# Kernel optimization log

Measured on AMD Instinct MI355X. Metric: run time of the kernel, lower is better.

The kernel has to match this reference:

```python
import jax, jax.numpy as jnp
import numpy as np

B, P, N, E, F = 1024, 64, 512, 256, 64

def setup_inputs() -> dict:
    key = jax.random.key(0)
    ks = jax.random.split(key, 10)
    return {
        'feasible_personal_info_nodes': jax.random.uniform(ks[0], (B, P), dtype=jnp.float32),
        'workers_decision': jax.random.uniform(ks[1], (B, P, 2), dtype=jnp.float32),
        'known_one_hot': jax.random.uniform(ks[2], (B, P, F), dtype=jnp.float32),
        'unknown_one_hot': jax.random.uniform(ks[3], (B, P, F), dtype=jnp.float32),
        'known_differ_one_hot': jax.random.uniform(ks[4], (B, P, F), dtype=jnp.float32),
        'total_qa_turn_one_hot': jax.random.uniform(ks[5], (B, F), dtype=jnp.float32),
        'personal_nodes': jax.random.randint(ks[6], (B, P), 0, N, dtype=jnp.int64) if jax.config.jax_enable_x64 else jax.random.randint(ks[6], (B, P), 0, N, dtype=jnp.int32),
        'final_node_embed': jax.random.normal(ks[7], (B, N, E), dtype=jnp.float32),
        'W': jax.random.normal(ks[8], (E, E), dtype=jnp.float32) * 0.02,
        'b': jax.random.normal(ks[9], (E,), dtype=jnp.float32) * 0.02,
    }

def reference(feasible_personal_info_nodes, workers_decision, known_one_hot,
              unknown_one_hot, known_differ_one_hot, total_qa_turn_one_hot,
              personal_nodes, final_node_embed, W, b):
    batch_size, personal_node_num = personal_nodes.shape
    # batch_embedding_lookup: gather node rows per batch -> (B, P, E)
    personal_node_embed = jnp.take_along_axis(
        final_node_embed, personal_nodes[:, :, None], axis=1)
    # Linear + Tanh
    transferred = jnp.tanh(jnp.einsum('bpe,ef->bpf', personal_node_embed, W) + b)
    # msg_agg == 'avg'
    agg_state = jnp.sum(transferred, axis=1) / personal_node_num
    manager_state = jnp.concatenate((
        feasible_personal_info_nodes,
        workers_decision.reshape(batch_size, -1),
        known_one_hot.reshape(batch_size, -1),
        unknown_one_hot.reshape(batch_size, -1),
        known_differ_one_hot.reshape(batch_size, -1),
        total_qa_turn_one_hot,
        agg_state), axis=1)
    return manager_state
```

## Files before the change

### kernel.cpp

```cpp
#include <hip/hip_runtime.h>
#include <hip/hip_bf16.h>
#include <math.h>

#define BB 1024
#define PP 64
#define NN 512
#define EE 256


#define LDA 264

typedef short bf16x8 __attribute__((ext_vector_type(8)));
typedef float f32x4  __attribute__((ext_vector_type(4)));

__device__ inline unsigned short f2bf(float x) {
    union { float f; unsigned int u; } v; v.f = x;
    unsigned int r = (v.u + 0x7FFFu + ((v.u >> 16) & 1u)) >> 16;
    return (unsigned short)r;
}

__global__ void wconv_kernel(const float* __restrict__ W,
                             unsigned short* __restrict__ Wt) {
    int i = blockIdx.x * blockDim.x + threadIdx.x;
    int k = i >> 8;
    int f = i & 255;
    int t = f >> 4;
    int c = k >> 5;
    int kk = k & 31;
    int lane = (kk >> 3) * 16 + (f & 15);
    int dst = (((t * 8 + c) * 64) + lane) * 8 + (kk & 7);
    Wt[dst] = f2bf(W[i]);
}

__global__ void fused_kernel(
    const float* __restrict__ feas, const float* __restrict__ workers,
    const float* __restrict__ known, const float* __restrict__ unknown,
    const float* __restrict__ differ, const float* __restrict__ qa,
    const int* __restrict__ pn, const float* __restrict__ embed,
    const float* __restrict__ bias, const unsigned short* __restrict__ Wt,
    float* __restrict__ out)
{
    if (blockIdx.x < BB) {
        __shared__ unsigned short sA[PP * LDA];
        const int b = blockIdx.x;
        const int tid = threadIdx.x;

        {
            const int p = tid >> 2, q = tid & 3;
            const int idx = pn[b * PP + p];
            const float4* src =
                (const float4*)(embed + ((size_t)b * NN + idx) * EE) + q * 16;
            unsigned short* dst = sA + p * LDA + q * 64;
            #pragma unroll
            for (int i = 0; i < 16; ++i) {
                float4 v = src[i];
                dst[i * 4 + 0] = f2bf(v.x);
                dst[i * 4 + 1] = f2bf(v.y);
                dst[i * 4 + 2] = f2bf(v.z);
                dst[i * 4 + 3] = f2bf(v.w);
            }
        }
        __syncthreads();

        const int wave = tid >> 6, lane = tid & 63;
        const int m = lane & 15, quad = lane >> 4;

        f32x4 acc[4][4];
        #pragma unroll
        for (int mt = 0; mt < 4; ++mt)
            #pragma unroll
            for (int ft = 0; ft < 4; ++ft)
                acc[mt][ft] = (f32x4){0.f, 0.f, 0.f, 0.f};

        #pragma unroll
        for (int c = 0; c < 8; ++c) {
            bf16x8 aF[4], bF[4];
            #pragma unroll
            for (int mt = 0; mt < 4; ++mt) {
                const unsigned short* ap =
                    sA + (mt * 16 + m) * LDA + c * 32 + quad * 8;
                aF[mt] = *(const bf16x8*)ap;
            }
            #pragma unroll
            for (int ft = 0; ft < 4; ++ft) {
                const int t = wave * 4 + ft;
                const unsigned short* bp = Wt + (((t * 8 + c) * 64) + lane) * 8;
                bF[ft] = *(const bf16x8*)bp;
            }
            #pragma unroll
            for (int mt = 0; mt < 4; ++mt)
                #pragma unroll
                for (int ft = 0; ft < 4; ++ft)
                    acc[mt][ft] = __builtin_amdgcn_mfma_f32_16x16x32_bf16(
                        aF[mt], bF[ft], acc[mt][ft], 0, 0, 0);
        }

        const float inv = 1.0f / 64.0f;
        #pragma unroll
        for (int ft = 0; ft < 4; ++ft) {
            const int f = wave * 64 + ft * 16 + m;
            const float bia = bias[f];
            float s = 0.f;
            #pragma unroll
            for (int mt = 0; mt < 4; ++mt)
                #pragma unroll
                for (int r = 0; r < 4; ++r)
                    s += tanhf(acc[mt][ft][r] + bia);
            s += __shfl_xor(s, 16, 64);
            s += __shfl_xor(s, 32, 64);
            if (quad == 0)
                out[(size_t)b * 12800 + 12544 + f] = s * inv;
        }
    } else {
        const int cid = blockIdx.x - BB;
        float4* out4 = (float4*)out;
        const float4* s_feas = (const float4*)feas;
        const float4* s_work = (const float4*)workers;
        const float4* s_know = (const float4*)known;
        const float4* s_unkn = (const float4*)unknown;
        const float4* s_diff = (const float4*)differ;
        const float4* s_qa   = (const float4*)qa;
        const int total = BB * 3136;
        for (int i = cid * 256 + threadIdx.x; i < total; i += BB * 256) {
            const int b = i / 3136;
            const int r = i - b * 3136;
            float4 v;
            if (r < 16)        v = s_feas[b * 16 + r];
            else if (r < 48)   v = s_work[b * 32 + (r - 16)];
            else if (r < 1072) v = s_know[(size_t)b * 1024 + (r - 48)];
            else if (r < 2096) v = s_unkn[(size_t)b * 1024 + (r - 1072)];
            else if (r < 3120) v = s_diff[(size_t)b * 1024 + (r - 2096)];
            else               v = s_qa[b * 16 + (r - 3120)];
            out4[(size_t)b * 3200 + r] = v;
        }
    }
}

extern "C" void kernel_launch(void* const* d_in, const int* in_sizes, int n_in,
                              void* d_out, int out_size, void* d_ws, size_t ws_size,
                              hipStream_t stream) {
    const float* feas    = (const float*)d_in[0];
    const float* workers = (const float*)d_in[1];
    const float* known   = (const float*)d_in[2];
    const float* unknown = (const float*)d_in[3];
    const float* differ  = (const float*)d_in[4];
    const float* qa      = (const float*)d_in[5];
    const int*   pn      = (const int*)d_in[6];
    const float* embed   = (const float*)d_in[7];
    const float* W       = (const float*)d_in[8];
    const float* bias    = (const float*)d_in[9];
    float* out = (float*)d_out;
    unsigned short* Wt = (unsigned short*)d_ws;

    wconv_kernel<<<256, 256, 0, stream>>>(W, Wt);
    fused_kernel<<<2 * BB, 256, 0, stream>>>(feas, workers, known, unknown,
                                             differ, qa, pn, embed, bias, Wt,
                                             out);
}
```

Measured before the change: 659.2 us.

## Merge concat copy into per-batch GEMM blocks and use fast tanh

```diff
diff --git a/kernel.cpp b/kernel.cpp
--- a/kernel.cpp
+++ b/kernel.cpp
@@ -1,5 +1,4 @@
 #include <hip/hip_runtime.h>
-#include <hip/hip_bf16.h>
 #include <math.h>
 
 #define BB 1024
@@ -11,12 +10,20 @@
 #define LDA 264
 
 typedef short bf16x8 __attribute__((ext_vector_type(8)));
+typedef short bf16x4 __attribute__((ext_vector_type(4)));
 typedef float f32x4  __attribute__((ext_vector_type(4)));
 
 __device__ inline unsigned short f2bf(float x) {
     union { float f; unsigned int u; } v; v.f = x;
     unsigned int r = (v.u + 0x7FFFu + ((v.u >> 16) & 1u)) >> 16;
     return (unsigned short)r;
+}
+
+__device__ inline float fast_tanh(float x) {
+    float ax = fabsf(x);
+    float e  = __expf(-2.0f * ax);
+    float y  = (1.0f - e) * __builtin_amdgcn_rcpf(1.0f + e);
+    return copysignf(y, x);
 }
 
 __global__ void wconv_kernel(const float* __restrict__ W,
@@ -32,7 +39,7 @@
     Wt[dst] = f2bf(W[i]);
 }
 
-__global__ void fused_kernel(
+__global__ __launch_bounds__(256, 4) void fused_kernel(
     const float* __restrict__ feas, const float* __restrict__ workers,
     const float* __restrict__ known, const float* __restrict__ unknown,
     const float* __restrict__ differ, const float* __restrict__ qa,
@@ -40,99 +47,95 @@
     const float* __restrict__ bias, const unsigned short* __restrict__ Wt,
     float* __restrict__ out)
 {
-    if (blockIdx.x < BB) {
-        __shared__ unsigned short sA[PP * LDA];
-        const int b = blockIdx.x;
-        const int tid = threadIdx.x;
+    __shared__ unsigned short sA[PP * LDA];
+    const int b = blockIdx.x;
+    const int tid = threadIdx.x;
+    const int wave = tid >> 6, lane = tid & 63;
 
-        {
-            const int p = tid >> 2, q = tid & 3;
-            const int idx = pn[b * PP + p];
-            const float4* src =
-                (const float4*)(embed + ((size_t)b * NN + idx) * EE) + q * 16;
-            unsigned short* dst = sA + p * LDA + q * 64;
-            #pragma unroll
-            for (int i = 0; i < 16; ++i) {
-                float4 v = src[i];
-                dst[i * 4 + 0] = f2bf(v.x);
-                dst[i * 4 + 1] = f2bf(v.y);
-                dst[i * 4 + 2] = f2bf(v.z);
-                dst[i * 4 + 3] = f2bf(v.w);
-            }
+    {
+        const int* pnb = pn + b * PP;
+        const float* ebase = embed + (size_t)b * NN * EE;
+        #pragma unroll
+        for (int i = 0; i < 16; ++i) {
+            const int p = wave * 16 + i;
+            const float4 v =
+                ((const float4*)(ebase + (size_t)pnb[p] * EE))[lane];
+            bf16x4 t;
+            t[0] = (short)f2bf(v.x);
+            t[1] = (short)f2bf(v.y);
+            t[2] = (short)f2bf(v.z);
+            t[3] = (short)f2bf(v.w);
+            *(bf16x4*)(sA + p * LDA + lane * 4) = t;
         }
-        __syncthreads();
+    }
 
-        const int wave = tid >> 6, lane = tid & 63;
-        const int m = lane & 15, quad = lane >> 4;
+    float4* out4 = (float4*)out + (size_t)b * 3200;
 
-        f32x4 acc[4][4];
+    if (tid < 64) {
+        if (tid < 16)      out4[tid]        = ((const float4*)feas)[b * 16 + tid];
+        else if (tid < 48) out4[tid]        = ((const float4*)workers)[b * 32 + tid - 16];
+        else               out4[3072 + tid] = ((const float4*)qa)[b * 16 + tid - 48];
+    }
+    {
+        const float4* s = (const float4*)known + (size_t)b * 1024;
+        #pragma unroll
+        for (int k = 0; k < 4; ++k)
+            out4[48 + k * 256 + tid] = s[k * 256 + tid];
+    }
+
+    __syncthreads();
+
+    const int m = lane & 15, quad = lane >> 4;
+    f32x4 acc[4][4];
+    #pragma unroll
+    for (int mt = 0; mt < 4; ++mt)
+        #pragma unroll
+        for (int ft = 0; ft < 4; ++ft)
+            acc[mt][ft] = (f32x4){0.f, 0.f, 0.f, 0.f};
+
+    #pragma unroll
+    for (int c = 0; c < 8; ++c) {
+        bf16x8 aF[4], bF[4];
+        #pragma unroll
+        for (int mt = 0; mt < 4; ++mt)
+            aF[mt] = *(const bf16x8*)(sA + (mt * 16 + m) * LDA + c * 32 + quad * 8);
+        #pragma unroll
+        for (int ft = 0; ft < 4; ++ft)
+            bF[ft] = *(const bf16x8*)(Wt + ((((wave * 4 + ft) * 8 + c) * 64) + lane) * 8);
         #pragma unroll
         for (int mt = 0; mt < 4; ++mt)
             #pragma unroll
             for (int ft = 0; ft < 4; ++ft)
-                acc[mt][ft] = (f32x4){0.f, 0.f, 0.f, 0.f};
+                acc[mt][ft] = __builtin_amdgcn_mfma_f32_16x16x32_bf16(
+                    aF[mt], bF[ft], acc[mt][ft], 0, 0, 0);
+    }
 
+    const float inv = 1.0f / 64.0f;
+    #pragma unroll
+    for (int ft = 0; ft < 4; ++ft) {
+        const int f = wave * 64 + ft * 16 + m;
+        const float bia = bias[f];
+        float s = 0.f;
         #pragma unroll
-        for (int c = 0; c < 8; ++c) {
-            bf16x8 aF[4], bF[4];
+        for (int mt = 0; mt < 4; ++mt)
             #pragma unroll
-            for (int mt = 0; mt < 4; ++mt) {
-                const unsigned short* ap =
-                    sA + (mt * 16 + m) * LDA + c * 32 + quad * 8;
-                aF[mt] = *(const bf16x8*)ap;
-            }
-            #pragma unroll
-            for (int ft = 0; ft < 4; ++ft) {
-                const int t = wave * 4 + ft;
-                const unsigned short* bp = Wt + (((t * 8 + c) * 64) + lane) * 8;
-                bF[ft] = *(const bf16x8*)bp;
-            }
-            #pragma unroll
-            for (int mt = 0; mt < 4; ++mt)
-                #pragma unroll
-                for (int ft = 0; ft < 4; ++ft)
-                    acc[mt][ft] = __builtin_amdgcn_mfma_f32_16x16x32_bf16(
-                        aF[mt], bF[ft], acc[mt][ft], 0, 0, 0);
-        }
+            for (int r = 0; r < 4; ++r)
+                s += fast_tanh(acc[mt][ft][r] + bia);
+        s += __shfl_xor(s, 16, 64);
+        s += __shfl_xor(s, 32, 64);
+        if (quad == 0)
+            out[(size_t)b * 12800 + 12544 + f] = s * inv;
+    }
 
-        const float inv = 1.0f / 64.0f;
+    {
+        const float4* su = (const float4*)unknown + (size_t)b * 1024;
+        const float4* sd = (const float4*)differ + (size_t)b * 1024;
         #pragma unroll
-        for (int ft = 0; ft < 4; ++ft) {
-            const int f = wave * 64 + ft * 16 + m;
-            const float bia = bias[f];
-            float s = 0.f;
-            #pragma unroll
-            for (int mt = 0; mt < 4; ++mt)
-                #pragma unroll
-                for (int r = 0; r < 4; ++r)
-                    s += tanhf(acc[mt][ft][r] + bia);
-            s += __shfl_xor(s, 16, 64);
-            s += __shfl_xor(s, 32, 64);
-            if (quad == 0)
-                out[(size_t)b * 12800 + 12544 + f] = s * inv;
-        }
-    } else {
-        const int cid = blockIdx.x - BB;
-        float4* out4 = (float4*)out;
-        const float4* s_feas = (const float4*)feas;
-        const float4* s_work = (const float4*)workers;
-        const float4* s_know = (const float4*)known;
-        const float4* s_unkn = (const float4*)unknown;
-        const float4* s_diff = (const float4*)differ;
-        const float4* s_qa   = (const float4*)qa;
-        const int total = BB * 3136;
-        for (int i = cid * 256 + threadIdx.x; i < total; i += BB * 256) {
-            const int b = i / 3136;
-            const int r = i - b * 3136;
-            float4 v;
-            if (r < 16)        v = s_feas[b * 16 + r];
-            else if (r < 48)   v = s_work[b * 32 + (r - 16)];
-            else if (r < 1072) v = s_know[(size_t)b * 1024 + (r - 48)];
-            else if (r < 2096) v = s_unkn[(size_t)b * 1024 + (r - 1072)];
-            else if (r < 3120) v = s_diff[(size_t)b * 1024 + (r - 2096)];
-            else               v = s_qa[b * 16 + (r - 3120)];
-            out4[(size_t)b * 3200 + r] = v;
-        }
+        for (int k = 0; k < 4; ++k)
+            out4[1072 + k * 256 + tid] = su[k * 256 + tid];
+        #pragma unroll
+        for (int k = 0; k < 4; ++k)
+            out4[2096 + k * 256 + tid] = sd[k * 256 + tid];
     }
 }
 
@@ -153,7 +156,7 @@
     unsigned short* Wt = (unsigned short*)d_ws;
 
     wconv_kernel<<<256, 256, 0, stream>>>(W, Wt);
-    fused_kernel<<<2 * BB, 256, 0, stream>>>(feas, workers, known, unknown,
-                                             differ, qa, pn, embed, bias, Wt,
-                                             out);
+    fused_kernel<<<BB, 256, 0, stream>>>(feas, workers, known, unknown,
+                                         differ, qa, pn, embed, bias, Wt,
+                                         out);
 }
```

Result: no change. 653.9 us (-0.8%).
